# Optimization experiments

Hardware: AMD Instinct MI355X
Metric: run time of the kernel (lower is better)

The kernel has to match this reference:

```python
import jax, jax.numpy as jnp
import numpy as np

N_NODES = 10000
N_EDGES = 70000
IN_DIM = 10
HEADS = 6
LIN_OUT = 254
GAT_DIMS = [(256, 508), (512, 250), (256, 120), (128, 20)]  # (in_dim, out_dim) per DeformGAT
NEG_SLOPE = 0.2


def setup_inputs() -> dict:
    key = jax.random.key(0)
    ks = jax.random.split(key, 8)
    inp = {}
    inp["data"] = jax.random.normal(ks[0], (N_NODES, IN_DIM), dtype=jnp.float32)
    inp["edge_idx"] = jax.random.randint(ks[1], (2, N_EDGES), 0, N_NODES)
    inp["bd_mask"] = jax.random.randint(ks[2], (N_NODES,), 0, 2) > 0
    inp["poly_mesh"] = 0
    inp["W_lin"] = jax.random.normal(ks[3], (IN_DIM, LIN_OUT), dtype=jnp.float32) * 0.05
    inp["b_lin"] = jnp.zeros((LIN_OUT,), dtype=jnp.float32)
    for i, (din, dout) in enumerate(GAT_DIMS):
        k1, k2, k3 = jax.random.split(ks[4 + i], 3)
        inp[f"W{i+1}"] = jax.random.normal(k1, (din, HEADS * dout), dtype=jnp.float32) * 0.05
        inp[f"asrc{i+1}"] = jax.random.normal(k2, (HEADS, dout), dtype=jnp.float32) * 0.05
        inp[f"adst{i+1}"] = jax.random.normal(k3, (HEADS, dout), dtype=jnp.float32) * 0.05
    return inp


def deform_gat(coord, feat, src, dst, bd_mask, W, a_src, a_dst, n):
    """One DeformGAT layer: GAT attention over edge list; features aggregated
    (head-averaged, SELU); coords moved to attention-weighted neighbor centroid,
    boundary nodes pinned."""
    H, C = a_src.shape
    x = (feat @ W).reshape(-1, H, C)                       # [N,H,C]
    a_s = jnp.einsum('nhc,hc->nh', x, a_src)               # [N,H]
    a_d = jnp.einsum('nhc,hc->nh', x, a_dst)               # [N,H]
    e = jax.nn.leaky_relu(a_s[src] + a_d[dst], NEG_SLOPE)  # [E,H]
    # segment softmax over incoming edges of each dst node
    m = jax.ops.segment_max(e, dst, num_segments=n)
    m = jnp.where(jnp.isfinite(m), m, 0.0)
    ex = jnp.exp(e - m[dst])
    denom = jax.ops.segment_sum(ex, dst, num_segments=n)
    alpha = ex / jnp.where(denom[dst] > 0, denom[dst], 1.0)        # [E,H]
    agg = jax.ops.segment_sum(alpha[:, :, None] * x[src], dst, num_segments=n)  # [N,H,C]
    out_feat = jax.nn.selu(agg.mean(axis=1))                       # [N,C]
    am = alpha.mean(axis=1)                                        # [E]
    new_coord = jax.ops.segment_sum(am[:, None] * coord[src], dst, num_segments=n)  # [N,2]
    out_coord = jnp.where(bd_mask[:, None], coord, new_coord)
    return out_coord, out_feat


def reference(data, edge_idx, bd_mask, poly_mesh, W_lin, b_lin,
              W1, asrc1, adst1, W2, asrc2, adst2,
              W3, asrc3, adst3, W4, asrc4, adst4):
    n = data.shape[0]
    coords = data[:, 0:2]
    src, dst = edge_idx[0], edge_idx[1]
    h = jax.nn.selu(data @ W_lin + b_lin)                  # [N,254]
    t1 = jnp.concatenate([coords, h], axis=1)              # [N,256]
    c1, f1 = deform_gat(coords, t1, src, dst, bd_mask, W1, asrc1, adst1, n)
    t2 = jnp.concatenate([c1, coords, f1], axis=1)         # [N,512]
    c2, f2 = deform_gat(c1, t2, src, dst, bd_mask, W2, asrc2, adst2, n)
    t3 = jnp.concatenate([c2, c1, coords, f2], axis=1)     # [N,256]
    c3, f3 = deform_gat(c2, t3, src, dst, bd_mask, W3, asrc3, adst3, n)
    t4 = jnp.concatenate([c3, c2, c1, coords, f3], axis=1) # [N,128]
    c4, f4 = deform_gat(c3, t4, src, dst, bd_mask, W4, asrc4, adst4, n)
    return c4
```

## Files before the change

### kernel.cpp

```cpp
#include <hip/hip_runtime.h>
#include <hip/hip_bf16.h>

#define N_NODES 10000
#define N_EDGES 70000
#define HEADS 6
#define MPAD 10112
#define SELU_SCALE 1.0507009873554805f
#define SELU_ALPHA  1.6732632423543772f
#define NEG_SLOPE 0.2f

typedef __attribute__((ext_vector_type(8))) __bf16 bf16x8;
typedef __attribute__((ext_vector_type(4))) float f32x4;

__device__ __forceinline__ float selu_f(float x) {
    return x > 0.f ? SELU_SCALE * x : SELU_SCALE * SELU_ALPHA * (__expf(x) - 1.f);
}
__device__ __forceinline__ unsigned short f2bf(float f) {
    __hip_bfloat16 h = __float2bfloat16(f);
    return __builtin_bit_cast(unsigned short, h);
}
__device__ __forceinline__ float bf2f(unsigned short u) {
    unsigned int x = ((unsigned int)u) << 16;
    return __builtin_bit_cast(float, x);
}

__global__ void count_edges_k(const int* __restrict__ dstv, int* __restrict__ counts) {
    int e = blockIdx.x * blockDim.x + threadIdx.x;
    if (e < N_EDGES) atomicAdd(&counts[dstv[e]], 1);
}

__global__ __launch_bounds__(1024) void scan_k(const int* __restrict__ counts, int* __restrict__ offs) {
    __shared__ int part[1024];
    int tid = threadIdx.x;
    const int per = (N_NODES + 1023) / 1024;
    int start = tid * per;
    int s = 0;
    for (int i = 0; i < per; ++i) { int idx = start + i; if (idx < N_NODES) s += counts[idx]; }
    part[tid] = s;
    __syncthreads();
    for (int off = 1; off < 1024; off <<= 1) {
        int v = (tid >= off) ? part[tid - off] : 0;
        __syncthreads();
        part[tid] += v;
        __syncthreads();
    }
    int run = part[tid] - s;
    for (int i = 0; i < per; ++i) {
        int idx = start + i;
        if (idx < N_NODES) { offs[idx] = run; run += counts[idx]; }
    }
    if (tid == 0) offs[N_NODES] = part[1023];
}

__global__ void fill_csr_k(const int* __restrict__ dstv, const int* __restrict__ offs,
                           int* __restrict__ cursor, int* __restrict__ csr) {
    int e = blockIdx.x * blockDim.x + threadIdx.x;
    if (e < N_EDGES) {
        int d = dstv[e];
        int pos = atomicAdd(&cursor[d], 1);
        csr[offs[d] + pos] = e;
    }
}

__global__ __launch_bounds__(256) void prep_k(const float* __restrict__ data,
                                              const float* __restrict__ W,
                                              const float* __restrict__ b,
                                              float* __restrict__ coords0,
                                              unsigned short* __restrict__ t1) {
    int idx = blockIdx.x * blockDim.x + threadIdx.x;
    if (idx >= N_NODES * 256) return;
    int n = idx >> 8, c = idx & 255;
    if (c < 2) {
        float v = data[n * 10 + c];
        t1[(size_t)n * 256 + c] = f2bf(v);
        if (c == 0) {
            coords0[2 * n] = data[n * 10];
            coords0[2 * n + 1] = data[n * 10 + 1];
        }
    } else {
        int cc = c - 2;
        float acc = b[cc];
        const float* dr = data + (size_t)n * 10;
#pragma unroll
        for (int k = 0; k < 10; ++k) acc += dr[k] * W[k * 254 + cc];
        t1[(size_t)n * 256 + c] = f2bf(selu_f(acc));
    }
}

__global__ __launch_bounds__(64) void fold_all_k(
    const float* __restrict__ W0, const float* __restrict__ s0v, const float* __restrict__ d0v,
    const float* __restrict__ W1, const float* __restrict__ s1v, const float* __restrict__ d1v,
    const float* __restrict__ W2, const float* __restrict__ s2v, const float* __restrict__ d2v,
    const float* __restrict__ W3, const float* __restrict__ s3v, const float* __restrict__ d3v,
    float* __restrict__ wsf0, float* __restrict__ wdf0,
    float* __restrict__ wsf1, float* __restrict__ wdf1,
    float* __restrict__ wsf2, float* __restrict__ wdf2,
    float* __restrict__ wsf3, float* __restrict__ wdf3) {
    int bid = blockIdx.x;
    const float* W; const float* sv; const float* dv; float* ws; float* wd;
    int K, C, pair;
    if (bid < 1536)      { W = W0; sv = s0v; dv = d0v; ws = wsf0; wd = wdf0; K = 256; C = 508; pair = bid; }
    else if (bid < 4608) { W = W1; sv = s1v; dv = d1v; ws = wsf1; wd = wdf1; K = 512; C = 250; pair = bid - 1536; }
    else if (bid < 6144) { W = W2; sv = s2v; dv = d2v; ws = wsf2; wd = wdf2; K = 256; C = 120; pair = bid - 4608; }
    else                 { W = W3; sv = s3v; dv = d3v; ws = wsf3; wd = wdf3; K = 128; C = 20;  pair = bid - 6144; }
    int k = pair / HEADS, h = pair % HEADS;
    int lane = threadIdx.x;
    const float* wr = W + (size_t)k * (HEADS * C) + h * C;
    const float* sr = sv + h * C;
    const float* dr = dv + h * C;
    float s = 0.f, d = 0.f;
    for (int c = lane; c < C; c += 64) {
        float w = wr[c];
        s += w * sr[c];
        d += w * dr[c];
    }
#pragma unroll
    for (int off = 32; off > 0; off >>= 1) {
        s += __shfl_xor(s, off);
        d += __shfl_xor(d, off);
    }
    if (lane == 0) { ws[pair] = s; wd[pair] = d; }
}

__global__ __launch_bounds__(256) void convv_all_k(
    const float* __restrict__ W0, unsigned short* __restrict__ Vt0,
    const float* __restrict__ W1, unsigned short* __restrict__ Vt1,
    const float* __restrict__ W2, unsigned short* __restrict__ Vt2) {
    __shared__ float tile[64][65];
    int bid = blockIdx.x;
    const float* W; unsigned short* Vt; int K, C, K6, bid2, ktiles;
    if (bid < 192)      { W = W0; Vt = Vt0; K = 256; C = 508; K6 = 1536; bid2 = bid;       ktiles = 24; }
    else if (bid < 384) { W = W1; Vt = Vt1; K = 512; C = 250; K6 = 3072; bid2 = bid - 192; ktiles = 48; }
    else                { W = W2; Vt = Vt2; K = 256; C = 120; K6 = 1536; bid2 = bid - 384; ktiles = 24; }
    int kb = bid2 % ktiles, cb = bid2 / ktiles;
    const int tx = threadIdx.x;
    const int ty = threadIdx.y;
    const int k0 = kb * 64;
    const int c0 = cb * 64;
    for (int i = ty; i < 64; i += 4) {
        int kk = k0 + i;
        int h = kk / K, k = kk - h * K;
        int c = c0 + tx;
        tile[i][tx] = (c < C) ? W[(size_t)k * (HEADS * C) + h * C + c] : 0.f;
    }
    __syncthreads();
    for (int i = ty; i < 64; i += 4) {
        int c = c0 + i;
        Vt[(size_t)c * K6 + k0 + tx] = f2bf(tile[tx][i]);
    }
}

__global__ __launch_bounds__(256) void gemm_split_k(
    const unsigned short* __restrict__ A,
    const unsigned short* __restrict__ Bt,
    unsigned short* __restrict__ part,
    int Kpitch, int klen, int Npad) {
    __shared__ unsigned short lds[16384];
    const int tid = threadIdx.x;
    const int lane = tid & 63, wid = tid >> 6;
    const int wm = wid >> 1, wn = wid & 1;
    const int m0 = blockIdx.y * 128;
    const int n0 = blockIdx.x * 128;
    const int kz = blockIdx.z;
    const int kbeg = kz * klen;

    f32x4 acc[4][4] = {};

    const unsigned short* gsrc[8];
    unsigned ldsoff[8];
#pragma unroll
    for (int i = 0; i < 8; ++i) {
        const int half = i >> 2;
        const int slot = (i & 3) * 256 + tid;
        const int r = slot >> 3;
        const int c16 = slot & 7;
        const int ksl = c16 ^ (r & 7);
        gsrc[i] = (half ? (Bt + (size_t)(n0 + r) * Kpitch) : (A + (size_t)(m0 + r) * Kpitch)) + ksl * 8;
        ldsoff[i] = (unsigned)(half * 8192 + ((i & 3) * 256 + wid * 64) * 8);
    }

    for (int kt = kbeg; kt < kbeg + klen; kt += 64) {
#pragma unroll
        for (int i = 0; i < 8; ++i) {
            __builtin_amdgcn_global_load_lds(
                (const __attribute__((address_space(1))) unsigned int*)(gsrc[i] + kt),
                (__attribute__((address_space(3))) unsigned int*)(&lds[ldsoff[i]]),
                16, 0, 0);
        }
        __syncthreads();
#pragma unroll
        for (int kc = 0; kc < 2; ++kc) {
            const int xo = (((kc * 4 + (lane >> 4)) ^ (lane & 7)) << 4);
            bf16x8 aop[4], bop[4];
#pragma unroll
            for (int f = 0; f < 4; ++f) {
                const int rA = wm * 64 + f * 16 + (lane & 15);
                bop[f] = *(const bf16x8*)((const char*)lds + rA * 128 + xo);
                const int rB = wn * 64 + f * 16 + (lane & 15);
                aop[f] = *(const bf16x8*)((const char*)lds + 16384 * 1 + rB * 128 + xo);
            }
#pragma unroll
            for (int fm = 0; fm < 4; ++fm)
#pragma unroll
                for (int fn = 0; fn < 4; ++fn)
                    acc[fm][fn] = __builtin_amdgcn_mfma_f32_16x16x32_bf16(
                        aop[fn], bop[fm], acc[fm][fn], 0, 0, 0);
        }
        __syncthreads();
    }

    unsigned short* pbase = part + (size_t)kz * MPAD * Npad;
    const int mrow = m0 + wm * 64 + (lane & 15);
    const int ncol = n0 + wn * 64 + ((lane >> 4) * 4);
#pragma unroll
    for (int fm = 0; fm < 4; ++fm) {
#pragma unroll
        for (int fn = 0; fn < 4; ++fn) {
            f32x4 v = acc[fm][fn];
            unsigned int u0 = (unsigned int)f2bf(v.x) | ((unsigned int)f2bf(v.y) << 16);
            unsigned int u1 = (unsigned int)f2bf(v.z) | ((unsigned int)f2bf(v.w) << 16);
            uint2 pk = make_uint2(u0, u1);
            *(uint2*)&pbase[(size_t)(mrow + fm * 16) * Npad + ncol + fn * 16] = pk;
        }
    }
}

__global__ __launch_bounds__(256) void reduce_feat_k(
    const unsigned short* __restrict__ part, unsigned short* __restrict__ tnext,
    int KS, int Npad, int ld, int off, int Cfeat) {
    int idx = blockIdx.x * 256 + threadIdx.x;
    int half = Npad >> 1;
    int r = idx / half, cp = idx - r * half;
    if (r >= N_NODES) return;
    int cb = cp * 2;
    if (cb >= Cfeat) return;
    const unsigned int* pp = (const unsigned int*)part;
    size_t stride = (size_t)MPAD * half;
    size_t base = (size_t)r * half + cp;
    float s0 = 0.f, s1 = 0.f;
    for (int kz = 0; kz < KS; ++kz) {
        unsigned int u = pp[kz * stride + base];
        s0 += bf2f((unsigned short)(u & 0xffff));
        s1 += bf2f((unsigned short)(u >> 16));
    }
    float o0 = selu_f(s0 * (1.f / 6.f));
    float o1 = selu_f(s1 * (1.f / 6.f));
    *(unsigned int*)&tnext[(size_t)r * ld + off + cb] =
        (unsigned int)f2bf(o0) | ((unsigned int)f2bf(o1) << 16);
}

__global__ __launch_bounds__(256) void proj2_k(const unsigned short* __restrict__ t,
                                               const float* __restrict__ wsf,
                                               const float* __restrict__ wdf,
                                               float* __restrict__ a_s,
                                               float* __restrict__ a_d, int K) {
    const int wv = threadIdx.x >> 6;
    const int lane = threadIdx.x & 63;
    const int n = blockIdx.x * 4 + wv;
    if (n >= N_NODES) return;
    const unsigned short* tr = t + (size_t)n * K;
    const int kpl = K >> 6;
    const int k0 = lane * kpl;

    unsigned int buf[4] = {0u, 0u, 0u, 0u};
    if (kpl == 8) {
        uint4 u = *(const uint4*)(tr + k0);
        buf[0] = u.x; buf[1] = u.y; buf[2] = u.z; buf[3] = u.w;
    } else if (kpl == 4) {
        uint2 u = *(const uint2*)(tr + k0);
        buf[0] = u.x; buf[1] = u.y;
    } else {
        buf[0] = *(const unsigned int*)(tr + k0);
    }

    float s[HEADS] = {}, d[HEADS] = {};
#pragma unroll
    for (int j = 0; j < 8; ++j) {
        if (j >= kpl) break;
        unsigned int w = buf[j >> 1];
        unsigned short u = (j & 1) ? (unsigned short)(w >> 16) : (unsigned short)(w & 0xffff);
        float v = bf2f(u);
        const float* ws = wsf + (size_t)(k0 + j) * HEADS;
        const float* wd = wdf + (size_t)(k0 + j) * HEADS;
#pragma unroll
        for (int h = 0; h < HEADS; ++h) {
            s[h] += v * ws[h];
            d[h] += v * wd[h];
        }
    }
#pragma unroll
    for (int off = 32; off > 0; off >>= 1) {
#pragma unroll
        for (int h = 0; h < HEADS; ++h) {
            s[h] += __shfl_xor(s[h], off);
            d[h] += __shfl_xor(d[h], off);
        }
    }
    if (lane == 0) {
#pragma unroll
        for (int h = 0; h < HEADS; ++h) {
            a_s[n * HEADS + h] = s[h];
            a_d[n * HEADS + h] = d[h];
        }
    }
}

__global__ __launch_bounds__(256) void attn_agg_move_k(
    const float* __restrict__ a_s, const float* __restrict__ a_d,
    const int* __restrict__ srcv, const int* __restrict__ csr,
    const int* __restrict__ offs,
    const unsigned short* __restrict__ t_in, unsigned short* __restrict__ thagg,
    int K,
    const float* __restrict__ cprev, const int* __restrict__ bd,
    float* __restrict__ cout, unsigned short* __restrict__ tnext, int ld,
    const float* __restrict__ xA, int offA,
    const float* __restrict__ xB, int offB) {
    const int n = blockIdx.x;
    const int tid = threadIdx.x;
    const int lane = tid & 63, w = tid >> 6;
    const int r0 = offs[n], r1 = offs[n + 1];

    __shared__ float m_sh[HEADS], rd_sh[HEADS], ad_sh[HEADS];
    __shared__ float al_sh[128][HEADS];
    __shared__ int src_sh[128];
    __shared__ float mrg[128][12];
    __shared__ float cxy_sh[2];

    for (int h = w; h < HEADS; h += 4) {
        float ad = a_d[n * HEADS + h];
        if (lane == 0) ad_sh[h] = ad;
        float m = -1e30f, s = 0.f;
        for (int i = r0 + lane; i < r1; i += 64) {
            float v = a_s[srcv[csr[i]] * HEADS + h] + ad;
            v = v > 0.f ? v : NEG_SLOPE * v;
            float nm = fmaxf(m, v);
            s = s * __expf(m - nm) + __expf(v - nm);
            m = nm;
        }
#pragma unroll
        for (int off = 32; off > 0; off >>= 1) {
            float mo = __shfl_xor(m, off);
            float so = __shfl_xor(s, off);
            float nm = fmaxf(m, mo);
            s = s * __expf(m - nm) + so * __expf(mo - nm);
            m = nm;
        }
        if (lane == 0) { m_sh[h] = m; rd_sh[h] = (s > 0.f) ? 1.f / s : 0.f; }
    }
    __syncthreads();

    float acc0[HEADS] = {}, acc1[HEADS] = {};
    float cx = 0.f, cy = 0.f;
    const int th = (K == 256) ? (tid & 127) : tid;
    const int eo = (K == 256) ? (tid >> 7) : 0;
    const int k0 = th * 2;
    for (int base = r0; base < r1; base += 128) {
        int cnt = min(128, r1 - base);
        if (tid < cnt) src_sh[tid] = srcv[csr[base + tid]];
        __syncthreads();
        for (int j = tid; j < cnt * HEADS; j += 256) {
            int i = j / HEADS, h = j - i * HEADS;
            float v = a_s[src_sh[i] * HEADS + h] + ad_sh[h];
            v = v > 0.f ? v : NEG_SLOPE * v;
            al_sh[i][h] = __expf(v - m_sh[h]) * rd_sh[h];
        }
        __syncthreads();
        if (K == 512) {
#pragma unroll 2
            for (int i = 0; i < cnt; ++i) {
                unsigned int u = *(const unsigned int*)(t_in + (size_t)src_sh[i] * 512 + k0);
                float v0 = bf2f((unsigned short)(u & 0xffff));
                float v1 = bf2f((unsigned short)(u >> 16));
#pragma unroll
                for (int h = 0; h < HEADS; ++h) {
                    float a = al_sh[i][h];
                    acc0[h] += a * v0;
                    acc1[h] += a * v1;
                }
            }
        } else if (K == 256) {
#pragma unroll 2
            for (int i = 0; i < cnt; i += 2) {
                int ie = i + eo;
                if (ie < cnt) {
                    unsigned int u = *(const unsigned int*)(t_in + (size_t)src_sh[ie] * 256 + k0);
                    float v0 = bf2f((unsigned short)(u & 0xffff));
                    float v1 = bf2f((unsigned short)(u >> 16));
#pragma unroll
                    for (int h = 0; h < HEADS; ++h) {
                        float a = al_sh[ie][h];
                        acc0[h] += a * v0;
                        acc1[h] += a * v1;
                    }
                }
            }
        }
        if (w == 3) {
            for (int i = lane; i < cnt; i += 64) {
                int s = src_sh[i];
                const float* al = al_sh[i];
                float am = (al[0] + al[1] + al[2] + al[3] + al[4] + al[5]) * (1.f / 6.f);
                cx += am * cprev[2 * s];
                cy += am * cprev[2 * s + 1];
            }
        }
        __syncthreads();
    }

    if (K == 512) {
#pragma unroll
        for (int h = 0; h < HEADS; ++h) {
            unsigned int pk = (unsigned int)f2bf(acc0[h]) | ((unsigned int)f2bf(acc1[h]) << 16);
            *(unsigned int*)(thagg + (size_t)n * 3072 + h * 512 + k0) = pk;
        }
    } else if (K == 256) {
        if (eo == 1) {
#pragma unroll
            for (int h = 0; h < HEADS; ++h) { mrg[th][h] = acc0[h]; mrg[th][h + 6] = acc1[h]; }
        }
        __syncthreads();
        if (eo == 0) {
#pragma unroll
            for (int h = 0; h < HEADS; ++h) {
                float s0 = acc0[h] + mrg[th][h];
                float s1 = acc1[h] + mrg[th][h + 6];
                unsigned int pk = (unsigned int)f2bf(s0) | ((unsigned int)f2bf(s1) << 16);
                *(unsigned int*)(thagg + (size_t)n * 1536 + h * 256 + k0) = pk;
            }
        }
    }
    if (w == 3) {
#pragma unroll
        for (int off = 32; off > 0; off >>= 1) {
            cx += __shfl_xor(cx, off);
            cy += __shfl_xor(cy, off);
        }
        if (lane == 0) { cxy_sh[0] = cx; cxy_sh[1] = cy; }
    }
    __syncthreads();
    if (tid == 0) {
        float px = cprev[2 * n], py = cprev[2 * n + 1];
        float ocx, ocy;
        if (bd[n] != 0) { ocx = px; ocy = py; }
        else { ocx = cxy_sh[0]; ocy = cxy_sh[1]; }
        cout[2 * n] = ocx; cout[2 * n + 1] = ocy;
        if (tnext) {
            unsigned short* row = tnext + (size_t)n * ld;
            row[0] = f2bf(ocx); row[1] = f2bf(ocy);
            row[2] = f2bf(px);  row[3] = f2bf(py);
            if (xA) { row[offA] = f2bf(xA[2 * n]); row[offA + 1] = f2bf(xA[2 * n + 1]); }
            if (xB) { row[offB] = f2bf(xB[2 * n]); row[offB + 1] = f2bf(xB[2 * n + 1]); }
        }
    }
}

static inline int cdiv(int a, int b) { return (a + b - 1) / b; }

extern "C" void kernel_launch(void* const* d_in, const int* in_sizes, int n_in,
                              void* d_out, int out_size, void* d_ws, size_t ws_size,
                              hipStream_t stream) {
    const float* data = (const float*)d_in[0];
    const int* eidx = (const int*)d_in[1];
    const int* bd = (const int*)d_in[2];
    const float* W_lin = (const float*)d_in[4];
    const float* b_lin = (const float*)d_in[5];
    const float* Wl[4]  = {(const float*)d_in[6],  (const float*)d_in[9],
                           (const float*)d_in[12], (const float*)d_in[15]};
    const float* Asrc[4] = {(const float*)d_in[7],  (const float*)d_in[10],
                            (const float*)d_in[13], (const float*)d_in[16]};
    const float* Adst[4] = {(const float*)d_in[8],  (const float*)d_in[11],
                            (const float*)d_in[14], (const float*)d_in[17]};
    const int Kd[4] = {256, 512, 256, 128};
    const int Cd[4] = {508, 250, 120, 20};
    const int Cpadd[4] = {512, 256, 128, 0};
    const int KSd[4] = {2, 4, 4, 0};

    const int* srcv = eidx;
    const int* dstv = eidx + N_EDGES;

    char* p = (char*)d_ws;
    auto alloc = [&](size_t bytes) -> void* {
        void* r = (void*)p;
        p += (bytes + 255) & ~(size_t)255;
        return r;
    };
    unsigned short* tb1 = (unsigned short*)alloc((size_t)MPAD * 256 * 2);
    unsigned short* tb2 = (unsigned short*)alloc((size_t)MPAD * 512 * 2);
    unsigned short* tb3 = (unsigned short*)alloc((size_t)MPAD * 256 * 2);
    unsigned short* tb4 = (unsigned short*)alloc((size_t)MPAD * 128 * 2);
    unsigned short* thagg = (unsigned short*)alloc((size_t)MPAD * 3072 * 2);
    unsigned short* VtL[3];
    VtL[0] = (unsigned short*)alloc((size_t)512 * 1536 * 2);
    VtL[1] = (unsigned short*)alloc((size_t)256 * 3072 * 2);
    VtL[2] = (unsigned short*)alloc((size_t)128 * 1536 * 2);
    unsigned short* partb = (unsigned short*)alloc((size_t)8 * MPAD * 256 * 2);
    float* coords0 = (float*)alloc((size_t)N_NODES * 2 * 4);
    float* c1 = (float*)alloc((size_t)N_NODES * 2 * 4);
    float* c2 = (float*)alloc((size_t)N_NODES * 2 * 4);
    float* c3 = (float*)alloc((size_t)N_NODES * 2 * 4);
    float* a_s = (float*)alloc((size_t)N_NODES * HEADS * 4);
    float* a_d = (float*)alloc((size_t)N_NODES * HEADS * 4);
    float* wsfL[4]; float* wdfL[4];
    wsfL[0] = (float*)alloc(1536 * 4); wdfL[0] = (float*)alloc(1536 * 4);
    wsfL[1] = (float*)alloc(3072 * 4); wdfL[1] = (float*)alloc(3072 * 4);
    wsfL[2] = (float*)alloc(1536 * 4); wdfL[2] = (float*)alloc(1536 * 4);
    wsfL[3] = (float*)alloc(768 * 4);  wdfL[3] = (float*)alloc(768 * 4);
    int* counts = (int*)alloc((size_t)N_NODES * 4);
    int* cursor = (int*)alloc((size_t)N_NODES * 4);
    int* offs = (int*)alloc((size_t)(N_NODES + 1) * 4);
    int* csr = (int*)alloc((size_t)N_EDGES * 4);

    hipMemsetAsync(counts, 0, (size_t)((char*)offs - (char*)counts), stream);
    count_edges_k<<<cdiv(N_EDGES, 256), 256, 0, stream>>>(dstv, counts);
    scan_k<<<1, 1024, 0, stream>>>(counts, offs);
    fill_csr_k<<<cdiv(N_EDGES, 256), 256, 0, stream>>>(dstv, offs, cursor, csr);

    prep_k<<<cdiv(N_NODES * 256, 256), 256, 0, stream>>>(data, W_lin, b_lin, coords0, tb1);
    fold_all_k<<<6912, 64, 0, stream>>>(
        Wl[0], Asrc[0], Adst[0], Wl[1], Asrc[1], Adst[1],
        Wl[2], Asrc[2], Adst[2], Wl[3], Asrc[3], Adst[3],
        wsfL[0], wdfL[0], wsfL[1], wdfL[1], wsfL[2], wdfL[2], wsfL[3], wdfL[3]);
    convv_all_k<<<432, dim3(64, 4), 0, stream>>>(Wl[0], VtL[0], Wl[1], VtL[1], Wl[2], VtL[2]);

    unsigned short* tin[4]   = {tb1, tb2, tb3, tb4};
    unsigned short* tnext[4] = {tb2, tb3, tb4, nullptr};
    int ldn[4]  = {512, 256, 128, 0};
    int foff[4] = {4, 6, 8, 0};
    float* cprev[4] = {coords0, c1, c2, c3};
    float* cout[4]  = {c1, c2, c3, (float*)d_out};
    const float* xAv[4] = {nullptr, coords0, c1, nullptr};
    int offAv[4] = {0, 4, 4, 0};
    const float* xBv[4] = {nullptr, nullptr, coords0, nullptr};
    int offBv[4] = {0, 0, 6, 0};

    for (int l = 0; l < 4; ++l) {
        int K = Kd[l], C = Cd[l], Cpad = Cpadd[l], KS = KSd[l];
        int K6 = K * HEADS;
        proj2_k<<<cdiv(N_NODES, 4), 256, 0, stream>>>(tin[l], wsfL[l], wdfL[l], a_s, a_d, K);

        attn_agg_move_k<<<N_NODES, 256, 0, stream>>>(
            a_s, a_d, srcv, csr, offs,
            tin[l], (l < 3) ? thagg : nullptr, (l < 3) ? K : 0,
            cprev[l], bd, cout[l], tnext[l], ldn[l],
            xAv[l], offAv[l], xBv[l], offBv[l]);

        if (l < 3) {
            int klen = K6 / KS;
            gemm_split_k<<<dim3(Cpad / 128, MPAD / 128, KS), 256, 0, stream>>>(
                thagg, VtL[l], partb, K6, klen, Cpad);
            reduce_feat_k<<<cdiv(MPAD * (Cpad / 2), 256), 256, 0, stream>>>(
                partb, tnext[l], KS, Cpad, ldn[l], foff[l], C);
        }
    }
}
```

Measured before the change: 372.3 us.

## Map one wavefront per node in attention aggregation, dropping shared memory and barriers

Rewrites the attention/aggregation kernel so each 64-lane wavefront handles one destination node instead of a 256-thread block per node. Softmax statistics for all heads are kept in registers and reduced with shuffles, neighbor indices are broadcast with shuffles, and attention weights are recomputed per edge instead of staged in shared memory. Feature rows are read with wider vector loads (8 or 4 bf16 per lane), and the K dimension is made a template parameter. This removes block-level syncs, shared memory traffic and idle threads on low-degree nodes, at the cost of redundant exp work per edge and more registers per thread.

Result: faster. 347.9 us (-6.5%).

```diff
diff --git a/kernel.cpp b/kernel.cpp
--- a/kernel.cpp
+++ b/kernel.cpp
@@ -305,144 +305,141 @@
     }
 }
 
+template<int KT>
 __global__ __launch_bounds__(256) void attn_agg_move_k(
     const float* __restrict__ a_s, const float* __restrict__ a_d,
     const int* __restrict__ srcv, const int* __restrict__ csr,
     const int* __restrict__ offs,
     const unsigned short* __restrict__ t_in, unsigned short* __restrict__ thagg,
-    int K,
     const float* __restrict__ cprev, const int* __restrict__ bd,
     float* __restrict__ cout, unsigned short* __restrict__ tnext, int ld,
     const float* __restrict__ xA, int offA,
     const float* __restrict__ xB, int offB) {
-    const int n = blockIdx.x;
-    const int tid = threadIdx.x;
-    const int lane = tid & 63, w = tid >> 6;
+    const int wid = threadIdx.x >> 6, lane = threadIdx.x & 63;
+    const int n = blockIdx.x * 4 + wid;
+    if (n >= N_NODES) return;
     const int r0 = offs[n], r1 = offs[n + 1];
 
-    __shared__ float m_sh[HEADS], rd_sh[HEADS], ad_sh[HEADS];
-    __shared__ float al_sh[128][HEADS];
-    __shared__ int src_sh[128];
-    __shared__ float mrg[128][12];
-    __shared__ float cxy_sh[2];
-
-    for (int h = w; h < HEADS; h += 4) {
-        float ad = a_d[n * HEADS + h];
-        if (lane == 0) ad_sh[h] = ad;
-        float m = -1e30f, s = 0.f;
-        for (int i = r0 + lane; i < r1; i += 64) {
-            float v = a_s[srcv[csr[i]] * HEADS + h] + ad;
-            v = v > 0.f ? v : NEG_SLOPE * v;
-            float nm = fmaxf(m, v);
-            s = s * __expf(m - nm) + __expf(v - nm);
-            m = nm;
-        }
-#pragma unroll
-        for (int off = 32; off > 0; off >>= 1) {
-            float mo = __shfl_xor(m, off);
-            float so = __shfl_xor(s, off);
-            float nm = fmaxf(m, mo);
-            s = s * __expf(m - nm) + so * __expf(mo - nm);
-            m = nm;
-        }
-        if (lane == 0) { m_sh[h] = m; rd_sh[h] = (s > 0.f) ? 1.f / s : 0.f; }
-    }
-    __syncthreads();
-
-    float acc0[HEADS] = {}, acc1[HEADS] = {};
+    float ad[HEADS], mm[HEADS], ss[HEADS];
+#pragma unroll
+    for (int h = 0; h < HEADS; ++h) {
+        ad[h] = a_d[n * HEADS + h];
+        mm[h] = -1e30f; ss[h] = 0.f;
+    }
+
+    for (int base = r0; base < r1; base += 64) {
+        int i = base + lane;
+        if (i < r1) {
+            int src = srcv[csr[i]];
+#pragma unroll
+            for (int h = 0; h < HEADS; ++h) {
+                float v = a_s[src * HEADS + h] + ad[h];
+                v = v > 0.f ? v : NEG_SLOPE * v;
+                float nm = fmaxf(mm[h], v);
+                ss[h] = ss[h] * __expf(mm[h] - nm) + __expf(v - nm);
+                mm[h] = nm;
+            }
+        }
+    }
+#pragma unroll
+    for (int off = 32; off > 0; off >>= 1) {
+#pragma unroll
+        for (int h = 0; h < HEADS; ++h) {
+            float mo = __shfl_xor(mm[h], off);
+            float so = __shfl_xor(ss[h], off);
+            float nm = fmaxf(mm[h], mo);
+            ss[h] = ss[h] * __expf(mm[h] - nm) + so * __expf(mo - nm);
+            mm[h] = nm;
+        }
+    }
+    float rd[HEADS];
+#pragma unroll
+    for (int h = 0; h < HEADS; ++h) rd[h] = ss[h] > 0.f ? 1.f / ss[h] : 0.f;
+
+    constexpr int KPL = (KT > 0) ? (KT / 64) : 1;
+    float acc[HEADS][KPL] = {};
     float cx = 0.f, cy = 0.f;
-    const int th = (K == 256) ? (tid & 127) : tid;
-    const int eo = (K == 256) ? (tid >> 7) : 0;
-    const int k0 = th * 2;
-    for (int base = r0; base < r1; base += 128) {
-        int cnt = min(128, r1 - base);
-        if (tid < cnt) src_sh[tid] = srcv[csr[base + tid]];
-        __syncthreads();
-        for (int j = tid; j < cnt * HEADS; j += 256) {
-            int i = j / HEADS, h = j - i * HEADS;
-            float v = a_s[src_sh[i] * HEADS + h] + ad_sh[h];
-            v = v > 0.f ? v : NEG_SLOPE * v;
-            al_sh[i][h] = __expf(v - m_sh[h]) * rd_sh[h];
-        }
-        __syncthreads();
-        if (K == 512) {
-#pragma unroll 2
-            for (int i = 0; i < cnt; ++i) {
-                unsigned int u = *(const unsigned int*)(t_in + (size_t)src_sh[i] * 512 + k0);
-                float v0 = bf2f((unsigned short)(u & 0xffff));
-                float v1 = bf2f((unsigned short)(u >> 16));
+    for (int base = r0; base < r1; base += 64) {
+        int i = base + lane;
+        bool ok = i < r1;
+        int mysrc = ok ? srcv[csr[i]] : 0;
+        if (ok) {
+            float am = 0.f;
+#pragma unroll
+            for (int h = 0; h < HEADS; ++h) {
+                float v = a_s[mysrc * HEADS + h] + ad[h];
+                v = v > 0.f ? v : NEG_SLOPE * v;
+                am += __expf(v - mm[h]) * rd[h];
+            }
+            am *= (1.f / 6.f);
+            cx += am * cprev[2 * mysrc];
+            cy += am * cprev[2 * mysrc + 1];
+        }
+        if constexpr (KT > 0) {
+            int cnt = min(64, r1 - base);
+            for (int j = 0; j < cnt; ++j) {
+                int src = __shfl(mysrc, j);
+                float al[HEADS];
 #pragma unroll
                 for (int h = 0; h < HEADS; ++h) {
-                    float a = al_sh[i][h];
-                    acc0[h] += a * v0;
-                    acc1[h] += a * v1;
+                    float v = a_s[src * HEADS + h] + ad[h];
+                    v = v > 0.f ? v : NEG_SLOPE * v;
+                    al[h] = __expf(v - mm[h]) * rd[h];
+                }
+                if constexpr (KT == 512) {
+                    uint4 u = *(const uint4*)(t_in + (size_t)src * 512 + lane * 8);
+                    float tv[8];
+                    tv[0] = bf2f((unsigned short)(u.x & 0xffff)); tv[1] = bf2f((unsigned short)(u.x >> 16));
+                    tv[2] = bf2f((unsigned short)(u.y & 0xffff)); tv[3] = bf2f((unsigned short)(u.y >> 16));
+                    tv[4] = bf2f((unsigned short)(u.z & 0xffff)); tv[5] = bf2f((unsigned short)(u.z >> 16));
+                    tv[6] = bf2f((unsigned short)(u.w & 0xffff)); tv[7] = bf2f((unsigned short)(u.w >> 16));
+#pragma unroll
+                    for (int h = 0; h < HEADS; ++h)
+#pragma unroll
+                        for (int q = 0; q < 8; ++q) acc[h][q] += al[h] * tv[q];
+                } else {
+                    uint2 u = *(const uint2*)(t_in + (size_t)src * 256 + lane * 4);
+                    float tv[4];
+                    tv[0] = bf2f((unsigned short)(u.x & 0xffff)); tv[1] = bf2f((unsigned short)(u.x >> 16));
+                    tv[2] = bf2f((unsigned short)(u.y & 0xffff)); tv[3] = bf2f((unsigned short)(u.y >> 16));
+#pragma unroll
+                    for (int h = 0; h < HEADS; ++h)
+#pragma unroll
+                        for (int q = 0; q < 4; ++q) acc[h][q] += al[h] * tv[q];
                 }
             }
-        } else if (K == 256) {
-#pragma unroll 2
-            for (int i = 0; i < cnt; i += 2) {
-                int ie = i + eo;
-                if (ie < cnt) {
-                    unsigned int u = *(const unsigned int*)(t_in + (size_t)src_sh[ie] * 256 + k0);
-                    float v0 = bf2f((unsigned short)(u & 0xffff));
-                    float v1 = bf2f((unsigned short)(u >> 16));
-#pragma unroll
-                    for (int h = 0; h < HEADS; ++h) {
-                        float a = al_sh[ie][h];
-                        acc0[h] += a * v0;
-                        acc1[h] += a * v1;
-                    }
-                }
-            }
-        }
-        if (w == 3) {
-            for (int i = lane; i < cnt; i += 64) {
-                int s = src_sh[i];
-                const float* al = al_sh[i];
-                float am = (al[0] + al[1] + al[2] + al[3] + al[4] + al[5]) * (1.f / 6.f);
-                cx += am * cprev[2 * s];
-                cy += am * cprev[2 * s + 1];
-            }
-        }
-        __syncthreads();
-    }
-
-    if (K == 512) {
+        }
+    }
+
+    if constexpr (KT == 512) {
 #pragma unroll
         for (int h = 0; h < HEADS; ++h) {
-            unsigned int pk = (unsigned int)f2bf(acc0[h]) | ((unsigned int)f2bf(acc1[h]) << 16);
-            *(unsigned int*)(thagg + (size_t)n * 3072 + h * 512 + k0) = pk;
-        }
-    } else if (K == 256) {
-        if (eo == 1) {
-#pragma unroll
-            for (int h = 0; h < HEADS; ++h) { mrg[th][h] = acc0[h]; mrg[th][h + 6] = acc1[h]; }
-        }
-        __syncthreads();
-        if (eo == 0) {
-#pragma unroll
-            for (int h = 0; h < HEADS; ++h) {
-                float s0 = acc0[h] + mrg[th][h];
-                float s1 = acc1[h] + mrg[th][h + 6];
-                unsigned int pk = (unsigned int)f2bf(s0) | ((unsigned int)f2bf(s1) << 16);
-                *(unsigned int*)(thagg + (size_t)n * 1536 + h * 256 + k0) = pk;
-            }
-        }
-    }
-    if (w == 3) {
-#pragma unroll
-        for (int off = 32; off > 0; off >>= 1) {
-            cx += __shfl_xor(cx, off);
-            cy += __shfl_xor(cy, off);
-        }
-        if (lane == 0) { cxy_sh[0] = cx; cxy_sh[1] = cy; }
-    }
-    __syncthreads();
-    if (tid == 0) {
+            uint4 pk;
+            pk.x = (unsigned int)f2bf(acc[h][0]) | ((unsigned int)f2bf(acc[h][1]) << 16);
+            pk.y = (unsigned int)f2bf(acc[h][2]) | ((unsigned int)f2bf(acc[h][3]) << 16);
+            pk.z = (unsigned int)f2bf(acc[h][4]) | ((unsigned int)f2bf(acc[h][5]) << 16);
+            pk.w = (unsigned int)f2bf(acc[h][6]) | ((unsigned int)f2bf(acc[h][7]) << 16);
+            *(uint4*)(thagg + (size_t)n * 3072 + h * 512 + lane * 8) = pk;
+        }
+    } else if constexpr (KT == 256) {
+#pragma unroll
+        for (int h = 0; h < HEADS; ++h) {
+            uint2 pk;
+            pk.x = (unsigned int)f2bf(acc[h][0]) | ((unsigned int)f2bf(acc[h][1]) << 16);
+            pk.y = (unsigned int)f2bf(acc[h][2]) | ((unsigned int)f2bf(acc[h][3]) << 16);
+            *(uint2*)(thagg + (size_t)n * 1536 + h * 256 + lane * 4) = pk;
+        }
+    }
+#pragma unroll
+    for (int off = 32; off > 0; off >>= 1) {
+        cx += __shfl_xor(cx, off);
+        cy += __shfl_xor(cy, off);
+    }
+    if (lane == 0) {
         float px = cprev[2 * n], py = cprev[2 * n + 1];
         float ocx, ocy;
         if (bd[n] != 0) { ocx = px; ocy = py; }
-        else { ocx = cxy_sh[0]; ocy = cxy_sh[1]; }
+        else { ocx = cx; ocy = cy; }
         cout[2 * n] = ocx; cout[2 * n + 1] = ocy;
         if (tnext) {
             unsigned short* row = tnext + (size_t)n * ld;
@@ -538,11 +535,22 @@
         int K6 = K * HEADS;
         proj2_k<<<cdiv(N_NODES, 4), 256, 0, stream>>>(tin[l], wsfL[l], wdfL[l], a_s, a_d, K);
 
-        attn_agg_move_k<<<N_NODES, 256, 0, stream>>>(
-            a_s, a_d, srcv, csr, offs,
-            tin[l], (l < 3) ? thagg : nullptr, (l < 3) ? K : 0,
-            cprev[l], bd, cout[l], tnext[l], ldn[l],
-            xAv[l], offAv[l], xBv[l], offBv[l]);
+        if (l == 3) {
+            attn_agg_move_k<0><<<cdiv(N_NODES, 4), 256, 0, stream>>>(
+                a_s, a_d, srcv, csr, offs, tin[l], nullptr,
+                cprev[l], bd, cout[l], tnext[l], ldn[l],
+                xAv[l], offAv[l], xBv[l], offBv[l]);
+        } else if (K == 512) {
+            attn_agg_move_k<512><<<cdiv(N_NODES, 4), 256, 0, stream>>>(
+                a_s, a_d, srcv, csr, offs, tin[l], thagg,
+                cprev[l], bd, cout[l], tnext[l], ldn[l],
+                xAv[l], offAv[l], xBv[l], offBv[l]);
+        } else {
+            attn_agg_move_k<256><<<cdiv(N_NODES, 4), 256, 0, stream>>>(
+                a_s, a_d, srcv, csr, offs, tin[l], thagg,
+                cprev[l], bd, cout[l], tnext[l], ldn[l],
+                xAv[l], offAv[l], xBv[l], offBv[l]);
+        }
 
         if (l < 3) {
             int klen = K6 / KS;
```
